# Kernel optimization log

Hardware: AMD Instinct MI355X
Metric: run time of the kernel (lower is better)

The kernel has to match this reference:

```python
import jax, jax.numpy as jnp
import numpy as np

B, N, C = 4, 4096, 1024
H, W = 16, 256
D = C // H  # 64 head_dim


def _rope(t, f):
    # t: (B, N, H, D), f: (N, D//2, 2) -> pairwise rotation on consecutive channel pairs
    tr = t.reshape(*t.shape[:-1], D // 2, 2)
    fc = f.reshape(1, N, 1, D // 2, 2)
    out = jnp.stack([
        tr[..., 0] * fc[..., 0] - tr[..., 1] * fc[..., 1],
        tr[..., 1] * fc[..., 0] + tr[..., 0] * fc[..., 1],
    ], axis=-1)
    return out.reshape(t.shape)


def setup_inputs() -> dict:
    key = jax.random.key(0)
    ks = jax.random.split(key, 4)
    x = jax.random.normal(ks[0], (B, N, C), dtype=jnp.float32)
    freqs_cis = jax.random.normal(ks[1], (N, D // 2, 2), dtype=jnp.float32)
    qkv_w = jax.random.normal(ks[2], (3 * C, C), dtype=jnp.float32) * (C ** -0.5)
    proj_w = jax.random.normal(ks[3], (C, C), dtype=jnp.float32) * (C ** -0.5)
    proj_b = jnp.zeros((C,), dtype=jnp.float32)
    return {"x": x, "freqs_cis": freqs_cis, "qkv_w": qkv_w, "proj_w": proj_w, "proj_b": proj_b}


def reference(x, freqs_cis, qkv_w, proj_w, proj_b):
    nW = N // W
    scale = D ** -0.5
    qkv = (x @ qkv_w.T).reshape(B, N, 3, H, D)
    q, k, v = qkv[:, :, 0], qkv[:, :, 1], qkv[:, :, 2]  # (B, N, H, D)
    q = _rope(q, freqs_cis)
    k = _rope(k, freqs_cis)
    # block-diagonal window attention: q_idx//W == kv_idx//W
    qw = q.transpose(0, 2, 1, 3).reshape(B, H, nW, W, D)
    kw = k.transpose(0, 2, 1, 3).reshape(B, H, nW, W, D)
    vw = v.transpose(0, 2, 1, 3).reshape(B, H, nW, W, D)
    scores = jnp.einsum('bhwqd,bhwkd->bhwqk', qw, kw) * scale
    attn = jax.nn.softmax(scores, axis=-1)
    out = jnp.einsum('bhwqk,bhwkd->bhwqd', attn, vw)
    out = out.reshape(B, H, N, D).transpose(0, 2, 1, 3).reshape(B, N, C)
    return out @ proj_w.T + proj_b
```

## Files before the change

kernel.cpp:

```cpp
#include <hip/hip_runtime.h>
#include <stdint.h>
#include <stddef.h>

typedef __bf16 bf16;
typedef __bf16 bf16x4 __attribute__((ext_vector_type(4)));
typedef __bf16 bf16x8 __attribute__((ext_vector_type(8)));
typedef float f32x4 __attribute__((ext_vector_type(4)));

#define MFMA(a, b, c) __builtin_amdgcn_mfma_f32_16x16x32_bf16(a, b, c, 0, 0, 0)

static constexpr int kB = 4, kN = 4096, kC = 1024, kH = 16, kD = 64;
static constexpr int kM = kB * kN;
static constexpr int kK = 1024;
static constexpr int kQKVN = 3072;

__device__ __forceinline__ void cp16(const void* g, void* l) {
  __builtin_amdgcn_global_load_lds(
      (const __attribute__((address_space(1))) void*)g,
      (__attribute__((address_space(3))) void*)l, 16, 0, 0);
}

__global__ __launch_bounds__(256) void cvt_bf16(const float* __restrict__ src,
                                                bf16* __restrict__ dst, int n4) {
  const int i = blockIdx.x * 256 + threadIdx.x;
  if (i < n4) {
    const float4 v = ((const float4*)src)[i];
    bf16x4 o = {(bf16)v.x, (bf16)v.y, (bf16)v.z, (bf16)v.w};
    *(bf16x4*)&dst[4 * i] = o;
  }
}

__device__ __forceinline__ bf16x8 rope8(bf16x8 t, bf16x8 f) {
  bf16x8 o;
#pragma unroll
  for (int p = 0; p < 4; ++p) {
    float t0 = (float)t[2 * p], t1 = (float)t[2 * p + 1];
    float f0 = (float)f[2 * p], f1 = (float)f[2 * p + 1];
    o[2 * p]     = (bf16)(t0 * f0 - t1 * f1);
    o[2 * p + 1] = (bf16)(t1 * f0 + t0 * f1);
  }
  return o;
}

template <int NOUT, bool BIAS, typename OutT>
__global__ __launch_bounds__(512, 2) void gemm_bt(const bf16* __restrict__ A,
                                                  const bf16* __restrict__ Bw,
                                                  const float* __restrict__ bias,
                                                  OutT* __restrict__ Cout) {
  __shared__ unsigned short As[2][2][8192];
  __shared__ unsigned short Bs[2][2][8192];
  const int tid = threadIdx.x;
  const int wave = tid >> 6, lane = tid & 63;
  const int q4 = lane >> 4, l16 = lane & 15;
  const int wr = wave >> 2, wc = wave & 3;

  const int nwg = gridDim.x * gridDim.y;
  int bid = blockIdx.y * gridDim.x + blockIdx.x;
  bid = (bid & 7) * (nwg >> 3) + (bid >> 3);
  const int bx = bid % gridDim.x, by = bid / gridDim.x;
  const int n0 = bx * 256, m0 = by * 256;

  constexpr int NT = kK / 64;

  f32x4 acc[8][4] = {};

  auto stageA = [&](int kt, int half) {
    const int buf = kt & 1;
#pragma unroll
    for (int i = 0; i < 2; ++i) {
      const int c = i * 512 + tid;
      const int ks = c >> 9, row = (c >> 2) & 127, s = c & 3;
      const int kb = ks * 4 + (s ^ ((row >> 1) & 3));
      cp16(A + (size_t)(m0 + half * 128 + row) * kK + kt * 64 + kb * 8,
           &As[buf][half][c * 8]);
    }
  };
  auto stageB = [&](int kt, int half) {
    const int buf = kt & 1;
#pragma unroll
    for (int i = 0; i < 2; ++i) {
      const int c = i * 512 + tid;
      const int ks = c >> 9, row = (c >> 2) & 127, s = c & 3;
      const int kb = ks * 4 + (s ^ ((row >> 1) & 3));
      cp16(Bw + (size_t)(n0 + half * 128 + row) * kK + kt * 64 + kb * 8,
           &Bs[buf][half][c * 8]);
    }
  };

  stageA(0, 0); stageA(0, 1); stageB(0, 0); stageB(0, 1); stageB(1, 0); stageB(1, 1);
  asm volatile("s_waitcnt vmcnt(4)\n\ts_barrier" ::: "memory");

  const int s8 = (q4 ^ ((l16 >> 1) & 3)) * 8;
  const int brow = (wc & 1) * 64;

  for (int t = 0; t < NT; ++t) {
    const int rb = t & 1;
    const unsigned short* Ab = &As[rb][wr][0];
    const unsigned short* Bb = &Bs[rb][wc >> 1][0];
    bf16x8 a[4][2], b[4][2];

#pragma unroll
    for (int i = 0; i < 4; ++i) {
      const int row = i * 16 + l16;
      a[i][0] = *(const bf16x8*)&Ab[row * 32 + s8];
      a[i][1] = *(const bf16x8*)&Ab[(128 + row) * 32 + s8];
    }
#pragma unroll
    for (int j = 0; j < 2; ++j) {
      const int row = brow + j * 16 + l16;
      b[j][0] = *(const bf16x8*)&Bb[row * 32 + s8];
      b[j][1] = *(const bf16x8*)&Bb[(128 + row) * 32 + s8];
    }
    if (t + 1 < NT) stageA(t + 1, 0);
    asm volatile("s_barrier" ::: "memory");
    __builtin_amdgcn_s_setprio(1);
#pragma unroll
    for (int i = 0; i < 4; ++i)
#pragma unroll
      for (int j = 0; j < 2; ++j)
#pragma unroll
        for (int ks = 0; ks < 2; ++ks)
          acc[i][j] = MFMA(a[i][ks], b[j][ks], acc[i][j]);
    __builtin_amdgcn_s_setprio(0);
    asm volatile("s_barrier" ::: "memory");

#pragma unroll
    for (int j = 2; j < 4; ++j) {
      const int row = brow + j * 16 + l16;
      b[j][0] = *(const bf16x8*)&Bb[row * 32 + s8];
      b[j][1] = *(const bf16x8*)&Bb[(128 + row) * 32 + s8];
    }
    if (t + 1 < NT) stageA(t + 1, 1);
    asm volatile("s_barrier" ::: "memory");
    __builtin_amdgcn_s_setprio(1);
#pragma unroll
    for (int i = 0; i < 4; ++i)
#pragma unroll
      for (int j = 2; j < 4; ++j)
#pragma unroll
        for (int ks = 0; ks < 2; ++ks)
          acc[i][j] = MFMA(a[i][ks], b[j][ks], acc[i][j]);
    __builtin_amdgcn_s_setprio(0);
    asm volatile("s_barrier" ::: "memory");

#pragma unroll
    for (int i = 0; i < 4; ++i) {
      const int row = (4 + i) * 16 + l16;
      a[i][0] = *(const bf16x8*)&Ab[row * 32 + s8];
      a[i][1] = *(const bf16x8*)&Ab[(128 + row) * 32 + s8];
    }
    if (t + 2 < NT) stageB(t + 2, 0);
    asm volatile("s_barrier" ::: "memory");
    __builtin_amdgcn_s_setprio(1);
#pragma unroll
    for (int i = 0; i < 4; ++i)
#pragma unroll
      for (int j = 0; j < 2; ++j)
#pragma unroll
        for (int ks = 0; ks < 2; ++ks)
          acc[4 + i][j] = MFMA(a[i][ks], b[j][ks], acc[4 + i][j]);
    __builtin_amdgcn_s_setprio(0);
    asm volatile("s_barrier" ::: "memory");

    if (t + 2 < NT) {
      stageB(t + 2, 1);
      asm volatile("s_waitcnt vmcnt(4)\n\ts_barrier" ::: "memory");
    } else {
      asm volatile("s_waitcnt vmcnt(0)\n\ts_barrier" ::: "memory");
    }
    __builtin_amdgcn_s_setprio(1);
#pragma unroll
    for (int i = 0; i < 4; ++i)
#pragma unroll
      for (int j = 2; j < 4; ++j)
#pragma unroll
        for (int ks = 0; ks < 2; ++ks)
          acc[4 + i][j] = MFMA(a[i][ks], b[j][ks], acc[4 + i][j]);
    __builtin_amdgcn_s_setprio(0);
    asm volatile("s_barrier" ::: "memory");
  }

#pragma unroll
  for (int i = 0; i < 8; ++i) {
    const int rowb = m0 + wr * 128 + i * 16 + q4 * 4;
#pragma unroll
    for (int j = 0; j < 4; ++j) {
      const int col = n0 + wc * 64 + j * 16 + l16;
      const float bv = BIAS ? bias[col] : 0.0f;
#pragma unroll
      for (int r = 0; r < 4; ++r)
        Cout[(size_t)(rowb + r) * NOUT + col] = (OutT)(acc[i][j][r] + bv);
    }
  }
}

__global__ __launch_bounds__(256) void attn_win(const bf16* __restrict__ qkv,
                                                const bf16* __restrict__ freqs,
                                                bf16* __restrict__ ob) {
  __shared__ unsigned short k8[128 * 8 * 8];
  __shared__ unsigned short v8[16 * 64 * 8];
  __shared__ unsigned short pT[4][16 * 128];

  const int bid = blockIdx.x;
  const int w = bid & 15, h = (bid >> 4) & 15, b = bid >> 8;
  const int n0 = w * 256;
  const int tid = threadIdx.x;
  const int wave = tid >> 6, lane = tid & 63;
  const int q4 = lane >> 4, l16 = lane & 15;
  const float scale = 0.125f;
  const int swz = (l16 & 7) << 4;
  const int kx = l16 & 7;
  char* const pw = (char*)&pT[wave][0];

  bf16x8 qf[4][2];
#pragma unroll
  for (int g = 0; g < 4; ++g) {
    const int n = n0 + wave * 64 + g * 16 + l16;
    const bf16* qrow = qkv + (size_t)(b * kN + n) * kQKVN + h * kD;
    const bf16* frow = freqs + (size_t)n * kD;
#pragma unroll
    for (int s = 0; s < 2; ++s) {
      const int d0 = s * 32 + q4 * 8;
      qf[g][s] = rope8(*(const bf16x8*)(qrow + d0), *(const bf16x8*)(frow + d0));
    }
  }

  f32x4 O[4][4] = {};
  float mrow[4], lrow[4];
#pragma unroll
  for (int g = 0; g < 4; ++g) { mrow[g] = -3.0e38f; lrow[g] = 0.0f; }

  for (int c = 0; c < 2; ++c) {
    const int nc = n0 + c * 128;
    __syncthreads();
#pragma unroll
    for (int i = 0; i < 4; ++i) {
      const int cid = i * 256 + tid;
      {
        const int tok = cid >> 3, db = cid & 7;
        const int n = nc + tok;
        const size_t base = (size_t)(b * kN + n) * kQKVN + h * kD + db * 8;
        bf16x8 kv = *(const bf16x8*)(qkv + base + kC);
        bf16x8 fv = *(const bf16x8*)(freqs + (size_t)n * kD + db * 8);
        *(bf16x8*)&k8[(tok * 8 + (db ^ (tok & 7))) * 8] = rope8(kv, fv);
      }
      {
        const int tok = cid & 127, db = cid >> 7;
        const int n = nc + tok;
        const size_t base = (size_t)(b * kN + n) * kQKVN + h * kD + db * 8;
        bf16x8 vv = *(const bf16x8*)(qkv + base + 2 * kC);
        const int tb = tok >> 3, sl = tok & 7;
#pragma unroll
        for (int e = 0; e < 8; ++e) {
          const int d = db * 8 + e;
          ((bf16*)v8)[((tb * 64) + (d ^ (tb & 7))) * 8 + sl] = vv[e];
        }
      }
    }
    __syncthreads();

#pragma unroll
    for (int g = 0; g < 4; ++g) {
      f32x4 S[8] = {};
#pragma unroll
      for (int j = 0; j < 8; ++j)
#pragma unroll
        for (int s = 0; s < 2; ++s) {
          const int tok = j * 16 + l16;
          bf16x8 kf = *(const bf16x8*)&k8[(tok * 8 + ((q4 + 4 * s) ^ kx)) * 8];
          S[j] = MFMA(kf, qf[g][s], S[j]);
        }
      float m0_ = -3.0e38f, m1_ = -3.0e38f, m2_ = -3.0e38f, m3_ = -3.0e38f;
#pragma unroll
      for (int j = 0; j < 8; ++j) {
        S[j][0] *= scale; S[j][1] *= scale; S[j][2] *= scale; S[j][3] *= scale;
        m0_ = fmaxf(m0_, S[j][0]); m1_ = fmaxf(m1_, S[j][1]);
        m2_ = fmaxf(m2_, S[j][2]); m3_ = fmaxf(m3_, S[j][3]);
      }
      float mx = fmaxf(fmaxf(m0_, m1_), fmaxf(m2_, m3_));
      mx = fmaxf(mx, __shfl_xor(mx, 16));
      mx = fmaxf(mx, __shfl_xor(mx, 32));
      const float mnew = fmaxf(mrow[g], mx);
      const float al = __expf(mrow[g] - mnew);
      mrow[g] = mnew;
      float s0 = 0.f, s1 = 0.f, s2 = 0.f, s3 = 0.f;
#pragma unroll
      for (int j = 0; j < 8; ++j) {
        S[j][0] = __expf(S[j][0] - mnew); s0 += S[j][0];
        S[j][1] = __expf(S[j][1] - mnew); s1 += S[j][1];
        S[j][2] = __expf(S[j][2] - mnew); s2 += S[j][2];
        S[j][3] = __expf(S[j][3] - mnew); s3 += S[j][3];
      }
      float sm = (s0 + s1) + (s2 + s3);
      sm += __shfl_xor(sm, 16);
      sm += __shfl_xor(sm, 32);
      lrow[g] = lrow[g] * al + sm;
      float alr[4];
#pragma unroll
      for (int r = 0; r < 4; ++r) alr[r] = __shfl(al, q4 * 4 + r);
#pragma unroll
      for (int jd = 0; jd < 4; ++jd)
#pragma unroll
        for (int r = 0; r < 4; ++r) O[g][jd][r] *= alr[r];
#pragma unroll
      for (int j = 0; j < 8; ++j) {
        bf16x4 pk = {(bf16)S[j][0], (bf16)S[j][1], (bf16)S[j][2], (bf16)S[j][3]};
        *(bf16x4*)(pw + l16 * 256 + ((j * 32 + q4 * 8) ^ swz)) = pk;
      }
      asm volatile("s_waitcnt lgkmcnt(0)" ::: "memory");
#pragma unroll
      for (int s4 = 0; s4 < 4; ++s4) {
        bf16x8 pf = *(const bf16x8*)(pw + l16 * 256 + ((s4 * 64 + q4 * 16) ^ swz));
        const int tb2 = q4 + 4 * s4;
#pragma unroll
        for (int jd = 0; jd < 4; ++jd) {
          const int d2 = (l16 + 16 * jd) ^ (tb2 & 7);
          bf16x8 vf = *(const bf16x8*)&v8[(tb2 * 64 + d2) * 8];
          O[g][jd] = MFMA(pf, vf, O[g][jd]);
        }
      }
      asm volatile("" ::: "memory");
    }
  }

#pragma unroll
  for (int g = 0; g < 4; ++g) {
    float lr[4];
#pragma unroll
    for (int r = 0; r < 4; ++r) lr[r] = __shfl(lrow[g], q4 * 4 + r);
    const int nb = n0 + wave * 64 + g * 16 + q4 * 4;
#pragma unroll
    for (int jd = 0; jd < 4; ++jd) {
      const int d = l16 + 16 * jd;
#pragma unroll
      for (int r = 0; r < 4; ++r) {
        const float v = O[g][jd][r] / lr[r];
        ob[(size_t)(b * kN + nb + r) * kC + h * kD + d] = (bf16)v;
      }
    }
  }
}

extern "C" void kernel_launch(void* const* d_in, const int* in_sizes, int n_in,
                              void* d_out, int out_size, void* d_ws, size_t ws_size,
                              hipStream_t stream) {
  (void)in_sizes; (void)n_in; (void)out_size; (void)ws_size;
  const float* x      = (const float*)d_in[0];
  const float* freqs  = (const float*)d_in[1];
  const float* qkv_w  = (const float*)d_in[2];
  const float* proj_w = (const float*)d_in[3];
  const float* proj_b = (const float*)d_in[4];
  float* out = (float*)d_out;

  bf16* qkv_buf = (bf16*)d_ws;
  bf16* shared  = qkv_buf + (size_t)kM * kQKVN;
  bf16* x_b     = shared;
  bf16* attn_b  = shared;
  bf16* qkvw_b  = shared + (size_t)kM * kC;
  bf16* projw_b = qkvw_b + (size_t)kQKVN * kC;
  bf16* freqs_b = projw_b + (size_t)kC * kC;

  cvt_bf16<<<(kM * kC / 4 + 255) / 256, 256, 0, stream>>>(x, x_b, kM * kC / 4);
  cvt_bf16<<<(kQKVN * kC / 4 + 255) / 256, 256, 0, stream>>>(qkv_w, qkvw_b, kQKVN * kC / 4);
  cvt_bf16<<<(kC * kC / 4 + 255) / 256, 256, 0, stream>>>(proj_w, projw_b, kC * kC / 4);
  cvt_bf16<<<(kN * kD / 4 + 255) / 256, 256, 0, stream>>>(freqs, freqs_b, kN * kD / 4);

  for (int d = 0; d < 3; ++d)
    gemm_bt<kQKVN, false, bf16><<<dim3(kC / 256, kM / 256), 512, 0, stream>>>(
        x_b, qkvw_b + (size_t)d * kC * kK, nullptr, qkv_buf + d * kC);
  attn_win<<<dim3(kB * kH * (kN / 256)), 256, 0, stream>>>(qkv_buf, freqs_b, attn_b);
  gemm_bt<kC, true, float><<<dim3(kC / 256, kM / 256), 512, 0, stream>>>(
      attn_b, projw_b, proj_b, out);
}
```

Baseline: 372.9 us.

## Merge QKV GEMM launches and pack two attention windows per block

The three per-slice QKV GEMM launches become one launch whose grid covers the full 3072 output columns. The attention kernel now runs 512 threads per block, with two independent 4-wave groups each handling one (batch, head, window) tile and owning separate K/V LDS buffers, which halves the grid. The aim is to cut launch overhead and give each block more concurrent waves, at the cost of more LDS per block and shared __syncthreads across both groups.

Result: slower. 402.8 us (+8.0%).

```diff
diff --git a/kernel.cpp b/kernel.cpp
--- a/kernel.cpp
+++ b/kernel.cpp
@@ -194,28 +194,32 @@
   }
 }
 
-__global__ __launch_bounds__(256) void attn_win(const bf16* __restrict__ qkv,
+__global__ __launch_bounds__(512) void attn_win(const bf16* __restrict__ qkv,
                                                 const bf16* __restrict__ freqs,
                                                 bf16* __restrict__ ob) {
-  __shared__ unsigned short k8[128 * 8 * 8];
-  __shared__ unsigned short v8[16 * 64 * 8];
-  __shared__ unsigned short pT[4][16 * 128];
-
-  const int bid = blockIdx.x;
-  const int w = bid & 15, h = (bid >> 4) & 15, b = bid >> 8;
-  const int n0 = w * 256;
+  __shared__ unsigned short k8[2][8192];
+  __shared__ unsigned short v8[2][8192];
+  __shared__ unsigned short pT[8][2048];
+
   const int tid = threadIdx.x;
   const int wave = tid >> 6, lane = tid & 63;
+  const int grp = wave >> 2, wv = wave & 3;
+  const int tid4 = tid & 255;
+  const int wid = blockIdx.x * 2 + grp;
+  const int w = wid & 15, h = (wid >> 4) & 15, b = wid >> 8;
+  const int n0 = w * 256;
   const int q4 = lane >> 4, l16 = lane & 15;
   const float scale = 0.125f;
   const int swz = (l16 & 7) << 4;
   const int kx = l16 & 7;
   char* const pw = (char*)&pT[wave][0];
+  unsigned short* const kg = &k8[grp][0];
+  unsigned short* const vg = &v8[grp][0];
 
   bf16x8 qf[4][2];
 #pragma unroll
   for (int g = 0; g < 4; ++g) {
-    const int n = n0 + wave * 64 + g * 16 + l16;
+    const int n = n0 + wv * 64 + g * 16 + l16;
     const bf16* qrow = qkv + (size_t)(b * kN + n) * kQKVN + h * kD;
     const bf16* frow = freqs + (size_t)n * kD;
 #pragma unroll
@@ -235,14 +239,14 @@
     __syncthreads();
 #pragma unroll
     for (int i = 0; i < 4; ++i) {
-      const int cid = i * 256 + tid;
+      const int cid = i * 256 + tid4;
       {
         const int tok = cid >> 3, db = cid & 7;
         const int n = nc + tok;
         const size_t base = (size_t)(b * kN + n) * kQKVN + h * kD + db * 8;
         bf16x8 kv = *(const bf16x8*)(qkv + base + kC);
         bf16x8 fv = *(const bf16x8*)(freqs + (size_t)n * kD + db * 8);
-        *(bf16x8*)&k8[(tok * 8 + (db ^ (tok & 7))) * 8] = rope8(kv, fv);
+        *(bf16x8*)&kg[(tok * 8 + (db ^ (tok & 7))) * 8] = rope8(kv, fv);
       }
       {
         const int tok = cid & 127, db = cid >> 7;
@@ -253,7 +257,7 @@
 #pragma unroll
         for (int e = 0; e < 8; ++e) {
           const int d = db * 8 + e;
-          ((bf16*)v8)[((tb * 64) + (d ^ (tb & 7))) * 8 + sl] = vv[e];
+          ((bf16*)vg)[((tb * 64) + (d ^ (tb & 7))) * 8 + sl] = vv[e];
         }
       }
     }
@@ -267,7 +271,7 @@
 #pragma unroll
         for (int s = 0; s < 2; ++s) {
           const int tok = j * 16 + l16;
-          bf16x8 kf = *(const bf16x8*)&k8[(tok * 8 + ((q4 + 4 * s) ^ kx)) * 8];
+          bf16x8 kf = *(const bf16x8*)&kg[(tok * 8 + ((q4 + 4 * s) ^ kx)) * 8];
           S[j] = MFMA(kf, qf[g][s], S[j]);
         }
       float m0_ = -3.0e38f, m1_ = -3.0e38f, m2_ = -3.0e38f, m3_ = -3.0e38f;
@@ -315,7 +319,7 @@
 #pragma unroll
         for (int jd = 0; jd < 4; ++jd) {
           const int d2 = (l16 + 16 * jd) ^ (tb2 & 7);
-          bf16x8 vf = *(const bf16x8*)&v8[(tb2 * 64 + d2) * 8];
+          bf16x8 vf = *(const bf16x8*)&vg[(tb2 * 64 + d2) * 8];
           O[g][jd] = MFMA(pf, vf, O[g][jd]);
         }
       }
@@ -328,7 +332,7 @@
     float lr[4];
 #pragma unroll
     for (int r = 0; r < 4; ++r) lr[r] = __shfl(lrow[g], q4 * 4 + r);
-    const int nb = n0 + wave * 64 + g * 16 + q4 * 4;
+    const int nb = n0 + wv * 64 + g * 16 + q4 * 4;
 #pragma unroll
     for (int jd = 0; jd < 4; ++jd) {
       const int d = l16 + 16 * jd;
@@ -365,10 +369,9 @@
   cvt_bf16<<<(kC * kC / 4 + 255) / 256, 256, 0, stream>>>(proj_w, projw_b, kC * kC / 4);
   cvt_bf16<<<(kN * kD / 4 + 255) / 256, 256, 0, stream>>>(freqs, freqs_b, kN * kD / 4);
 
-  for (int d = 0; d < 3; ++d)
-    gemm_bt<kQKVN, false, bf16><<<dim3(kC / 256, kM / 256), 512, 0, stream>>>(
-        x_b, qkvw_b + (size_t)d * kC * kK, nullptr, qkv_buf + d * kC);
-  attn_win<<<dim3(kB * kH * (kN / 256)), 256, 0, stream>>>(qkv_buf, freqs_b, attn_b);
+  gemm_bt<kQKVN, false, bf16><<<dim3(kQKVN / 256, kM / 256), 512, 0, stream>>>(
+      x_b, qkvw_b, nullptr, qkv_buf);
+  attn_win<<<dim3(kB * kH * (kN / 256) / 2), 512, 0, stream>>>(qkv_buf, freqs_b, attn_b);
   gemm_bt<kC, true, float><<<dim3(kC / 256, kM / 256), 512, 0, stream>>>(
       attn_b, projw_b, proj_b, out);
 }
```
